# Kernel optimization log

Hardware: AMD Instinct MI355X
Metric: run time of the kernel (lower is better)

Reference implementation:

```python
import jax, jax.numpy as jnp
import numpy as np
import math

D = 1024
DFF = 4 * D
EPS = 1e-5

def layer_norm(x, g, b):
    mu = jnp.mean(x, axis=-1, keepdims=True)
    var = jnp.mean(jnp.square(x - mu), axis=-1, keepdims=True)
    return (x - mu) * jax.lax.rsqrt(var + EPS) * g + b

def setup_inputs() -> dict:
    key = jax.random.key(0)
    ks = jax.random.split(key, 12)
    s = 1.0 / math.sqrt(D)
    x = jax.random.normal(ks[0], (4, 2048, D), dtype=jnp.float32)
    Wq = jax.random.uniform(ks[1], (D, D), jnp.float32, -s, s)
    Wk = jax.random.uniform(ks[2], (D, D), jnp.float32, -s, s)
    Wv = jax.random.uniform(ks[3], (D, D), jnp.float32, -s, s)
    ln1_g = jnp.ones((D,), jnp.float32); ln1_b = jnp.zeros((D,), jnp.float32)
    ln2_g = jnp.ones((D,), jnp.float32); ln2_b = jnp.zeros((D,), jnp.float32)
    ff1_w = jax.random.uniform(ks[4], (D, DFF), jnp.float32, -s, s)
    ff1_b = jax.random.uniform(ks[5], (DFF,), jnp.float32, -s, s)
    s2 = 1.0 / math.sqrt(DFF)
    ff2_w = jax.random.uniform(ks[6], (DFF, D), jnp.float32, -s2, s2)
    ff2_b = jax.random.uniform(ks[7], (D,), jnp.float32, -s2, s2)
    return {"x": x, "Wq": Wq, "Wk": Wk, "Wv": Wv,
            "ln1_g": ln1_g, "ln1_b": ln1_b, "ln2_g": ln2_g, "ln2_b": ln2_b,
            "ff1_w": ff1_w, "ff1_b": ff1_b, "ff2_w": ff2_w, "ff2_b": ff2_b}

def reference(x, Wq, Wk, Wv, ln1_g, ln1_b, ln2_g, ln2_b, ff1_w, ff1_b, ff2_w, ff2_b):
    B, S, d = x.shape
    Q = x @ Wq  # [B,S,D]
    K = x @ Wk
    V = x @ Wv
    scores = jnp.einsum('bsd,btd->bst', Q, K) / math.sqrt(d)
    causal = jnp.tril(jnp.ones((S, S), dtype=bool))  # [S,S]
    scores = jnp.where(causal, scores, -jnp.inf)
    attn = jax.nn.softmax(scores, axis=-1)
    attn_out = jnp.einsum('bst,btd->bsd', attn, V)
    h = layer_norm(x + attn_out, ln1_g, ln1_b)
    ff = (jax.nn.gelu(h @ ff1_w + ff1_b, approximate=False)) @ ff2_w + ff2_b
    return layer_norm(h + ff, ln2_g, ln2_b)
```

## Files before the change

kernel.cpp:

```cpp
#include <hip/hip_runtime.h>
#include <math.h>


#define D_MODEL 1024
#define DFF_    4096
#define SEQ_    2048
#define NBATCH  4

typedef unsigned short u16;
typedef __attribute__((ext_vector_type(8))) short bf16x8;
typedef __attribute__((ext_vector_type(4))) float f32x4;

__device__ __forceinline__ u16 f2bf(float f) {
    unsigned u = __float_as_uint(f);
    unsigned r = (u + 0x7fffu + ((u >> 16) & 1u)) >> 16;
    return (u16)r;
}
__device__ __forceinline__ float bf2f(u16 h) {
    return __uint_as_float(((unsigned)h) << 16);
}

__device__ __forceinline__ void gld_lds16(const void* g, void* l) {
#if __has_builtin(__builtin_amdgcn_global_load_lds)
    typedef __attribute__((address_space(1))) const unsigned int as1_u32;
    typedef __attribute__((address_space(3))) unsigned int as3_u32;
    __builtin_amdgcn_global_load_lds((as1_u32*)g, (as3_u32*)l, 16, 0, 0);
#else
    *(bf16x8*)l = *(const bf16x8*)g;
#endif
}

constexpr int BMt = 128, BNt = 128, BKt = 32;

template <int CAUSAL, int EPI, int OUT, int SWZ_HS>
__global__ __launch_bounds__(256)
void mfma_gemm(const u16* __restrict__ Ah, const u16* __restrict__ Al,
               const u16* __restrict__ Bh, const u16* __restrict__ Bl,
               float* __restrict__ Cf, u16* __restrict__ Ch, u16* __restrict__ Cl,
               const float* __restrict__ bias, const float* __restrict__ resid,
               int M, int N, int K, long bA, long bB, long bC, float alpha)
{
    const int z = blockIdx.z;
    int bx = blockIdx.x, by = blockIdx.y;
    if (SWZ_HS > 0) {
        const int GX = gridDim.x, GY = gridDim.y;
        const int g   = bx + GX * by;
        const int xcd = g & 7;
        const int li  = g >> 3;
        const int RB  = GY >> 3;
        const int r   = li % SWZ_HS;
        const int c   = (li / SWZ_HS) % GX;
        const int s   = li / (SWZ_HS * GX);
        by = xcd * RB + s * SWZ_HS + r;
        bx = c;
    }
    const int rowStart = by * BMt;
    const int colStart = bx * BNt;
    if (CAUSAL == 1 && colStart >= rowStart + BMt) return;

    const u16* Ah_ = Ah + bA * z;
    const u16* Al_ = Al + bA * z;
    const u16* Bh_ = Bh + bB * z;
    const u16* Bl_ = Bl + bB * z;

    __shared__ __align__(16) u16 AsH[128][32];
    __shared__ __align__(16) u16 AsL[128][32];
    __shared__ __align__(16) u16 BsH[128][32];
    __shared__ __align__(16) u16 BsL[128][32];

    const int tid = threadIdx.x;
    const int l   = tid & 63;
    const int w   = tid >> 6;
    const int wr  = w >> 1, wc = w & 1;
    const int fr  = l & 15;
    const int fk  = (l >> 4) * 8;

    const f32x4 fz = {0.f, 0.f, 0.f, 0.f};
    f32x4 acc[4][4];
#pragma unroll
    for (int m = 0; m < 4; ++m)
#pragma unroll
        for (int n = 0; n < 4; ++n) acc[m][n] = fz;

    int kTiles = K / BKt;
    if (CAUSAL == 2) {
        int kEnd = rowStart + BMt;
        if (kEnd > K) kEnd = K;
        kTiles = kEnd / BKt;
    }

    for (int t = 0; t < kTiles; ++t) {
        const int kb = t * BKt;
#pragma unroll
        for (int s = 0; s < 2; ++s) {
            int gg = s * 256 + tid;
            int r  = gg >> 2;
            int ko = (gg & 3) * 8;
            size_t aoff = (size_t)(rowStart + r) * K + kb + ko;
            size_t boff = (size_t)(colStart + r) * K + kb + ko;
            gld_lds16(Ah_ + aoff, &AsH[0][0] + (size_t)gg * 8);
            gld_lds16(Al_ + aoff, &AsL[0][0] + (size_t)gg * 8);
            gld_lds16(Bh_ + boff, &BsH[0][0] + (size_t)gg * 8);
            gld_lds16(Bl_ + boff, &BsL[0][0] + (size_t)gg * 8);
        }
        __syncthreads();

        bf16x8 aH[4], aL[4], bH[4], bL[4];
#pragma unroll
        for (int m = 0; m < 4; ++m) {
            aH[m] = *(const bf16x8*)&AsH[wr * 64 + m * 16 + fr][fk];
            aL[m] = *(const bf16x8*)&AsL[wr * 64 + m * 16 + fr][fk];
        }
#pragma unroll
        for (int n = 0; n < 4; ++n) {
            bH[n] = *(const bf16x8*)&BsH[wc * 64 + n * 16 + fr][fk];
            bL[n] = *(const bf16x8*)&BsL[wc * 64 + n * 16 + fr][fk];
        }
#pragma unroll
        for (int m = 0; m < 4; ++m)
#pragma unroll
            for (int n = 0; n < 4; ++n) {
                acc[m][n] = __builtin_amdgcn_mfma_f32_16x16x32_bf16(aH[m], bH[n], acc[m][n], 0, 0, 0);
                acc[m][n] = __builtin_amdgcn_mfma_f32_16x16x32_bf16(aH[m], bL[n], acc[m][n], 0, 0, 0);
                acc[m][n] = __builtin_amdgcn_mfma_f32_16x16x32_bf16(aL[m], bH[n], acc[m][n], 0, 0, 0);
            }
        __syncthreads();
    }

#pragma unroll
    for (int m = 0; m < 4; ++m) {
#pragma unroll
        for (int n = 0; n < 4; ++n) {
            const int col = colStart + wc * 64 + n * 16 + fr;
            float bv = 0.f;
            if (EPI >= 1) bv = bias[col];
#pragma unroll
            for (int r = 0; r < 4; ++r) {
                const int row = rowStart + wr * 64 + m * 16 + (l >> 4) * 4 + r;
                float v = acc[m][n][r] * alpha;
                if (EPI >= 1) v += bv;
                if (EPI == 2) v = 0.5f * v * (1.0f + erff(v * 0.70710678118654752f));
                if (EPI == 3) v += resid[(size_t)row * N + col];
                if (OUT == 0) {
                    Cf[bC * z + (size_t)row * N + col] = v;
                } else if (OUT == 1) {
                    size_t o = bC * z + (size_t)row * N + col;
                    u16 h = f2bf(v);
                    Ch[o] = h;
                    Cl[o] = f2bf(v - bf2f(h));
                } else {
                    int b = row >> 11, tt = row & (SEQ_ - 1);
                    size_t o = ((size_t)b << 21) + ((size_t)col << 11) + tt;
                    u16 h = f2bf(v);
                    Ch[o] = h;
                    Cl[o] = f2bf(v - bf2f(h));
                }
            }
        }
    }
}

__global__ __launch_bounds__(256)
void split_f32(const float* __restrict__ in, u16* __restrict__ oh, u16* __restrict__ ol, long n4)
{
    long i  = (long)blockIdx.x * 256 + threadIdx.x;
    long st = (long)gridDim.x * 256;
    for (; i < n4; i += st) {
        float4 v = ((const float4*)in)[i];
        ushort4 h, lo;
        h.x = f2bf(v.x); lo.x = f2bf(v.x - bf2f(h.x));
        h.y = f2bf(v.y); lo.y = f2bf(v.y - bf2f(h.y));
        h.z = f2bf(v.z); lo.z = f2bf(v.z - bf2f(h.z));
        h.w = f2bf(v.w); lo.w = f2bf(v.w - bf2f(h.w));
        ((ushort4*)oh)[i] = h;
        ((ushort4*)ol)[i] = lo;
    }
}

__global__ __launch_bounds__(256)
void transpose_split(const float* __restrict__ in, u16* __restrict__ oh, u16* __restrict__ ol,
                     int R, int C)
{
    __shared__ float t[32][33];
    const int c0 = blockIdx.x * 32, r0 = blockIdx.y * 32;
    const int tx = threadIdx.x, ty = threadIdx.y;
#pragma unroll
    for (int s = 0; s < 4; ++s)
        t[ty + s * 8][tx] = in[(size_t)(r0 + ty + s * 8) * C + c0 + tx];
    __syncthreads();
#pragma unroll
    for (int s = 0; s < 4; ++s) {
        int cl = ty + s * 8;
        float v = t[tx][cl];
        size_t o = (size_t)(c0 + cl) * R + r0 + tx;
        u16 h = f2bf(v);
        oh[o] = h;
        ol[o] = f2bf(v - bf2f(h));
    }
}

__global__ __launch_bounds__(256)
void softmax_split(u16* __restrict__ hi, u16* __restrict__ lo)
{
    const int row = blockIdx.x;
    const int b   = row >> 11;
    const int i   = row & (SEQ_ - 1);
    u16* ph = hi + ((size_t)b * SEQ_ + i) * SEQ_;
    u16* pl = lo + ((size_t)b * SEQ_ + i) * SEQ_;
    const int len = i + 1;
    const int lenPad = (len + 127) & ~127;
    const int tid = threadIdx.x;
    __shared__ float buf[SEQ_];
    __shared__ float red[256];

    float m = -INFINITY;
    for (int j = tid; j < len; j += 256) {
        float s = bf2f(ph[j]) + bf2f(pl[j]);
        buf[j] = s;
        m = fmaxf(m, s);
    }
    red[tid] = m; __syncthreads();
    for (int o = 128; o > 0; o >>= 1) { if (tid < o) red[tid] = fmaxf(red[tid], red[tid + o]); __syncthreads(); }
    m = red[0]; __syncthreads();

    float sum = 0.f;
    for (int j = tid; j < len; j += 256) { float e = expf(buf[j] - m); buf[j] = e; sum += e; }
    red[tid] = sum; __syncthreads();
    for (int o = 128; o > 0; o >>= 1) { if (tid < o) red[tid] += red[tid + o]; __syncthreads(); }
    const float inv = 1.0f / red[0];

    for (int j = tid; j < len; j += 256) {
        float p = buf[j] * inv;
        u16 h = f2bf(p);
        ph[j] = h;
        pl[j] = f2bf(p - bf2f(h));
    }
    for (int j = len + tid; j < lenPad; j += 256) { ph[j] = 0; pl[j] = 0; }
}

__global__ __launch_bounds__(256)
void ln_kernel(const float* __restrict__ a, const float* __restrict__ r,
               const float* __restrict__ g, const float* __restrict__ beta,
               float* __restrict__ out, u16* __restrict__ oh, u16* __restrict__ ol)
{
    const int row = blockIdx.x, tid = threadIdx.x;
    float4 v = ((const float4*)(a + (size_t)row * D_MODEL))[tid];
    if (r) {
        float4 wv = ((const float4*)(r + (size_t)row * D_MODEL))[tid];
        v.x += wv.x; v.y += wv.y; v.z += wv.z; v.w += wv.w;
    }
    __shared__ float red[256];
    red[tid] = v.x + v.y + v.z + v.w; __syncthreads();
    for (int o = 128; o > 0; o >>= 1) { if (tid < o) red[tid] += red[tid + o]; __syncthreads(); }
    const float mu = red[0] * (1.0f / D_MODEL);
    __syncthreads();
    const float dx = v.x - mu, dy = v.y - mu, dz = v.z - mu, dw = v.w - mu;
    red[tid] = dx * dx + dy * dy + dz * dz + dw * dw; __syncthreads();
    for (int o = 128; o > 0; o >>= 1) { if (tid < o) red[tid] += red[tid + o]; __syncthreads(); }
    const float rs = rsqrtf(red[0] * (1.0f / D_MODEL) + 1e-5f);
    const float4 gv = ((const float4*)g)[tid];
    const float4 bv = ((const float4*)beta)[tid];
    float4 o4 = make_float4(dx * rs * gv.x + bv.x, dy * rs * gv.y + bv.y,
                            dz * rs * gv.z + bv.z, dw * rs * gv.w + bv.w);
    ((float4*)(out + (size_t)row * D_MODEL))[tid] = o4;
    if (oh) {
        ushort4 h, lo;
        h.x = f2bf(o4.x); lo.x = f2bf(o4.x - bf2f(h.x));
        h.y = f2bf(o4.y); lo.y = f2bf(o4.y - bf2f(h.y));
        h.z = f2bf(o4.z); lo.z = f2bf(o4.z - bf2f(h.z));
        h.w = f2bf(o4.w); lo.w = f2bf(o4.w - bf2f(h.w));
        ((ushort4*)(oh + (size_t)row * D_MODEL))[tid] = h;
        ((ushort4*)(ol + (size_t)row * D_MODEL))[tid] = lo;
    }
}

extern "C" void kernel_launch(void* const* d_in, const int* in_sizes, int n_in,
                              void* d_out, int out_size, void* d_ws, size_t ws_size,
                              hipStream_t stream)
{
    const float* x    = (const float*)d_in[0];
    const float* Wq   = (const float*)d_in[1];
    const float* Wk   = (const float*)d_in[2];
    const float* Wv   = (const float*)d_in[3];
    const float* ln1g = (const float*)d_in[4];
    const float* ln1b = (const float*)d_in[5];
    const float* ln2g = (const float*)d_in[6];
    const float* ln2b = (const float*)d_in[7];
    const float* W1   = (const float*)d_in[8];
    const float* b1   = (const float*)d_in[9];
    const float* W2   = (const float*)d_in[10];
    const float* b2   = (const float*)d_in[11];

    const int Mrows = NBATCH * SEQ_;

    char* wsb = (char*)d_ws;
    auto U = [&](size_t mb) { return (u16*)(wsb + mb * (size_t)(1 << 20)); };
    u16 *WqTh = U(0),   *WqTl = U(2);
    u16 *WkTh = U(4),   *WkTl = U(6);
    u16 *WvTh = U(8),   *WvTl = U(10);
    u16 *xsh  = U(12),  *xsl  = U(28);
    float* attn = (float*)(wsb + 12 * (size_t)(1 << 20));
    u16 *W1Th = U(12),  *W1Tl = U(20);
    u16 *W2Th = U(28),  *W2Tl = U(36);
    u16 *Qsh  = U(44),  *Qsl  = U(60);
    u16 *hsh  = U(44),  *hsl  = U(60);
    u16 *Ksh  = U(76),  *Ksl  = U(92);
    u16 *Vth  = U(108), *Vtl  = U(124);
    u16 *Ssh  = U(140), *Ssl  = U(172);
    u16 *fh   = U(76),  *fl   = U(140);
    float* h  = (float*)d_out;

    dim3 b256(256), tb(32, 8);

    transpose_split<<<dim3(32, 32), tb, 0, stream>>>(Wq, WqTh, WqTl, 1024, 1024);
    transpose_split<<<dim3(32, 32), tb, 0, stream>>>(Wk, WkTh, WkTl, 1024, 1024);
    transpose_split<<<dim3(32, 32), tb, 0, stream>>>(Wv, WvTh, WvTl, 1024, 1024);
    split_f32<<<dim3(2048), b256, 0, stream>>>(x, xsh, xsl, (long)Mrows * D_MODEL / 4);

    mfma_gemm<0, 0, 1, 4><<<dim3(8, 64, 1), b256, 0, stream>>>(
        xsh, xsl, WqTh, WqTl, nullptr, Qsh, Qsl, nullptr, nullptr,
        Mrows, D_MODEL, D_MODEL, 0, 0, 0, 1.f);
    mfma_gemm<0, 0, 1, 4><<<dim3(8, 64, 1), b256, 0, stream>>>(
        xsh, xsl, WkTh, WkTl, nullptr, Ksh, Ksl, nullptr, nullptr,
        Mrows, D_MODEL, D_MODEL, 0, 0, 0, 1.f);
    mfma_gemm<0, 0, 2, 4><<<dim3(8, 64, 1), b256, 0, stream>>>(
        xsh, xsl, WvTh, WvTl, nullptr, Vth, Vtl, nullptr, nullptr,
        Mrows, D_MODEL, D_MODEL, 0, 0, 0, 1.f);

    mfma_gemm<1, 0, 1, 0><<<dim3(16, 16, NBATCH), b256, 0, stream>>>(
        Qsh, Qsl, Ksh, Ksl, nullptr, Ssh, Ssl, nullptr, nullptr,
        SEQ_, SEQ_, D_MODEL, (long)SEQ_ * D_MODEL, (long)SEQ_ * D_MODEL,
        (long)SEQ_ * SEQ_, 0.03125f);
    softmax_split<<<dim3(Mrows), b256, 0, stream>>>(Ssh, Ssl);

    mfma_gemm<2, 0, 0, 0><<<dim3(8, 16, NBATCH), b256, 0, stream>>>(
        Ssh, Ssl, Vth, Vtl, attn, nullptr, nullptr, nullptr, nullptr,
        SEQ_, D_MODEL, SEQ_, (long)SEQ_ * SEQ_, (long)D_MODEL * SEQ_,
        (long)SEQ_ * D_MODEL, 1.f);

    ln_kernel<<<dim3(Mrows), b256, 0, stream>>>(x, attn, ln1g, ln1b, h, hsh, hsl);

    transpose_split<<<dim3(128, 32), tb, 0, stream>>>(W1, W1Th, W1Tl, 1024, 4096);
    transpose_split<<<dim3(32, 128), tb, 0, stream>>>(W2, W2Th, W2Tl, 4096, 1024);

    mfma_gemm<0, 2, 1, 4><<<dim3(32, 64, 1), b256, 0, stream>>>(
        hsh, hsl, W1Th, W1Tl, nullptr, fh, fl, b1, nullptr,
        Mrows, DFF_, D_MODEL, 0, 0, 0, 1.f);

    mfma_gemm<0, 3, 0, 1><<<dim3(8, 64, 1), b256, 0, stream>>>(
        fh, fl, W2Th, W2Tl, (float*)d_out, nullptr, nullptr, b2, h,
        Mrows, D_MODEL, DFF_, 0, 0, 0, 1.f);

    ln_kernel<<<dim3(Mrows), b256, 0, stream>>>(
        (const float*)d_out, nullptr, ln2g, ln2b, (float*)d_out, nullptr, nullptr);
}
```

Baseline: 1.038 ms.

## Add 512-thread 128x256 triple-buffered ping-pong GEMM for projection and FFN matmuls

Adds a new GEMM kernel with 512 threads, 128x256 tiles, and a three-stage LDS ring filled by direct global-to-LDS loads. Each K step is split into two halves whose staging is interleaved with MFMA bursts under raised wave priority. The kernel replaces the old GEMM for the Q/K/V projections and both FFN matmuls, aiming to hide memory latency and raise MFMA utilisation. It uses 144KB of LDS with two blocks per CU requested, which risks limiting occupancy and adds barrier overhead.

Result: faster. 949.8 us (-8.5%).

```diff
diff --git a/kernel.cpp b/kernel.cpp
--- a/kernel.cpp
+++ b/kernel.cpp
@@ -48,11 +48,11 @@
         const int xcd = g & 7;
         const int li  = g >> 3;
         const int RB  = GY >> 3;
-        const int r   = li % SWZ_HS;
-        const int c   = (li / SWZ_HS) % GX;
-        const int s   = li / (SWZ_HS * GX);
-        by = xcd * RB + s * SWZ_HS + r;
-        bx = c;
+        const int rr_ = li % SWZ_HS;
+        const int cc_ = (li / SWZ_HS) % GX;
+        const int ss_ = li / (SWZ_HS * GX);
+        by = xcd * RB + ss_ * SWZ_HS + rr_;
+        bx = cc_;
     }
     const int rowStart = by * BMt;
     const int colStart = bx * BNt;
@@ -145,6 +145,174 @@
                     Cf[bC * z + (size_t)row * N + col] = v;
                 } else if (OUT == 1) {
                     size_t o = bC * z + (size_t)row * N + col;
+                    u16 h = f2bf(v);
+                    Ch[o] = h;
+                    Cl[o] = f2bf(v - bf2f(h));
+                } else {
+                    int b = row >> 11, tt = row & (SEQ_ - 1);
+                    size_t o = ((size_t)b << 21) + ((size_t)col << 11) + tt;
+                    u16 h = f2bf(v);
+                    Ch[o] = h;
+                    Cl[o] = f2bf(v - bf2f(h));
+                }
+            }
+        }
+    }
+}
+
+template <int EPI, int OUT, int SWZ_HS>
+__global__ __launch_bounds__(512, 2)
+void mfma_gemm_ps(const u16* __restrict__ Ah, const u16* __restrict__ Al,
+                  const u16* __restrict__ Bh, const u16* __restrict__ Bl,
+                  float* __restrict__ Cf, u16* __restrict__ Ch, u16* __restrict__ Cl,
+                  const float* __restrict__ bias, const float* __restrict__ resid,
+                  int M, int N, int K, float alpha)
+{
+    int bx = blockIdx.x, by = blockIdx.y;
+    if (SWZ_HS > 0) {
+        const int GX = gridDim.x, GY = gridDim.y;
+        const int g   = bx + GX * by;
+        const int xcd = g & 7;
+        const int li  = g >> 3;
+        const int RB  = GY >> 3;
+        const int rr_ = li % SWZ_HS;
+        const int cc_ = (li / SWZ_HS) % GX;
+        const int ss_ = li / (SWZ_HS * GX);
+        by = xcd * RB + ss_ * SWZ_HS + rr_;
+        bx = cc_;
+    }
+    const int rowStart = by * 128;
+    const int colStart = bx * 256;
+
+    __shared__ __align__(16) char lds[3 * 49152];
+
+    const int tid = threadIdx.x;
+    const int l  = tid & 63;
+    const int w  = tid >> 6;
+    const int wr = w >> 2;
+    const int wc = w & 3;
+    const int fr = l & 15;
+    const int ck = l >> 4;
+
+    const int T = K >> 5;
+
+    const f32x4 fz = {0.f, 0.f, 0.f, 0.f};
+    f32x4 acc[4][4];
+#pragma unroll
+    for (int m = 0; m < 4; ++m)
+#pragma unroll
+        for (int n = 0; n < 4; ++n) acc[m][n] = fz;
+
+    auto stage_g = [&](const u16* __restrict__ src, int rowBase, int g,
+                       char* region, int kb) {
+        int row = g >> 2, cp = g & 3;
+        int ko  = (cp ^ ((row >> 1) & 3)) << 3;
+        gld_lds16(src + (size_t)(rowBase + row) * K + kb + ko, region + g * 16);
+    };
+    auto rd = [&](const char* region, int row) -> bf16x8 {
+        return *(const bf16x8*)(region + row * 64 + ((ck ^ ((row >> 1) & 3)) << 4));
+    };
+
+    {
+        char* b0 = lds;
+        char* b1 = lds + 49152;
+        stage_g(Ah, rowStart, tid,       b0 + 0,     0);
+        stage_g(Al, rowStart, tid,       b0 + 8192,  0);
+        stage_g(Bh, colStart, tid,       b0 + 16384, 0);
+        stage_g(Bh, colStart, tid + 512, b0 + 16384, 0);
+        stage_g(Bl, colStart, tid,       b0 + 32768, 0);
+        stage_g(Bl, colStart, tid + 512, b0 + 32768, 0);
+        stage_g(Ah, rowStart, tid,       b1 + 0,     32);
+        stage_g(Al, rowStart, tid,       b1 + 8192,  32);
+        stage_g(Bh, colStart, tid,       b1 + 16384, 32);
+        stage_g(Bh, colStart, tid + 512, b1 + 16384, 32);
+        stage_g(Bl, colStart, tid,       b1 + 32768, 32);
+        stage_g(Bl, colStart, tid + 512, b1 + 32768, 32);
+    }
+    asm volatile("s_waitcnt vmcnt(6)" ::: "memory");
+    __builtin_amdgcn_s_barrier();
+
+    for (int t = 0; t < T; ++t) {
+        const char* cb = lds + (t % 3) * 49152;
+        char*       sb = lds + ((t + 2) % 3) * 49152;
+        const bool  doStage = (t + 2) < T;
+        const int   kb2 = (t + 2) << 5;
+
+        bf16x8 aH[4], aL[4];
+#pragma unroll
+        for (int m = 0; m < 4; ++m) {
+            aH[m] = rd(cb + 0,    wr * 64 + m * 16 + fr);
+            aL[m] = rd(cb + 8192, wr * 64 + m * 16 + fr);
+        }
+        bf16x8 bH0 = rd(cb + 16384, wc * 64 + 0 * 16 + fr);
+        bf16x8 bH1 = rd(cb + 16384, wc * 64 + 1 * 16 + fr);
+        bf16x8 bL0 = rd(cb + 32768, wc * 64 + 0 * 16 + fr);
+        bf16x8 bL1 = rd(cb + 32768, wc * 64 + 1 * 16 + fr);
+        if (doStage) {
+            stage_g(Ah, rowStart, tid, sb + 0,     kb2);
+            stage_g(Al, rowStart, tid, sb + 8192,  kb2);
+            stage_g(Bh, colStart, tid, sb + 16384, kb2);
+        }
+        __builtin_amdgcn_s_barrier();
+        asm volatile("s_waitcnt lgkmcnt(0)" ::: "memory");
+        __builtin_amdgcn_s_setprio(1);
+#pragma unroll
+        for (int m = 0; m < 4; ++m) {
+            acc[m][0] = __builtin_amdgcn_mfma_f32_16x16x32_bf16(aH[m], bH0, acc[m][0], 0, 0, 0);
+            acc[m][0] = __builtin_amdgcn_mfma_f32_16x16x32_bf16(aH[m], bL0, acc[m][0], 0, 0, 0);
+            acc[m][0] = __builtin_amdgcn_mfma_f32_16x16x32_bf16(aL[m], bH0, acc[m][0], 0, 0, 0);
+            acc[m][1] = __builtin_amdgcn_mfma_f32_16x16x32_bf16(aH[m], bH1, acc[m][1], 0, 0, 0);
+            acc[m][1] = __builtin_amdgcn_mfma_f32_16x16x32_bf16(aH[m], bL1, acc[m][1], 0, 0, 0);
+            acc[m][1] = __builtin_amdgcn_mfma_f32_16x16x32_bf16(aL[m], bH1, acc[m][1], 0, 0, 0);
+        }
+        __builtin_amdgcn_s_setprio(0);
+        __builtin_amdgcn_s_barrier();
+
+        bf16x8 bH2 = rd(cb + 16384, wc * 64 + 2 * 16 + fr);
+        bf16x8 bH3 = rd(cb + 16384, wc * 64 + 3 * 16 + fr);
+        bf16x8 bL2 = rd(cb + 32768, wc * 64 + 2 * 16 + fr);
+        bf16x8 bL3 = rd(cb + 32768, wc * 64 + 3 * 16 + fr);
+        if (doStage) {
+            stage_g(Bh, colStart, tid + 512, sb + 16384, kb2);
+            stage_g(Bl, colStart, tid,       sb + 32768, kb2);
+            stage_g(Bl, colStart, tid + 512, sb + 32768, kb2);
+        }
+        __builtin_amdgcn_s_barrier();
+        asm volatile("s_waitcnt lgkmcnt(0)" ::: "memory");
+        __builtin_amdgcn_s_setprio(1);
+#pragma unroll
+        for (int m = 0; m < 4; ++m) {
+            acc[m][2] = __builtin_amdgcn_mfma_f32_16x16x32_bf16(aH[m], bH2, acc[m][2], 0, 0, 0);
+            acc[m][2] = __builtin_amdgcn_mfma_f32_16x16x32_bf16(aH[m], bL2, acc[m][2], 0, 0, 0);
+            acc[m][2] = __builtin_amdgcn_mfma_f32_16x16x32_bf16(aL[m], bH2, acc[m][2], 0, 0, 0);
+            acc[m][3] = __builtin_amdgcn_mfma_f32_16x16x32_bf16(aH[m], bH3, acc[m][3], 0, 0, 0);
+            acc[m][3] = __builtin_amdgcn_mfma_f32_16x16x32_bf16(aH[m], bL3, acc[m][3], 0, 0, 0);
+            acc[m][3] = __builtin_amdgcn_mfma_f32_16x16x32_bf16(aL[m], bH3, acc[m][3], 0, 0, 0);
+        }
+        __builtin_amdgcn_s_setprio(0);
+        if (doStage) asm volatile("s_waitcnt vmcnt(6)" ::: "memory");
+        else         asm volatile("s_waitcnt vmcnt(0)" ::: "memory");
+        __builtin_amdgcn_s_barrier();
+    }
+
+#pragma unroll
+    for (int m = 0; m < 4; ++m) {
+#pragma unroll
+        for (int n = 0; n < 4; ++n) {
+            const int col = colStart + wc * 64 + n * 16 + fr;
+            float bv = 0.f;
+            if (EPI >= 1) bv = bias[col];
+#pragma unroll
+            for (int rr = 0; rr < 4; ++rr) {
+                const int row = rowStart + wr * 64 + m * 16 + (l >> 4) * 4 + rr;
+                float v = acc[m][n][rr] * alpha;
+                if (EPI >= 1) v += bv;
+                if (EPI == 2) v = 0.5f * v * (1.0f + erff(v * 0.70710678118654752f));
+                if (EPI == 3) v += resid[(size_t)row * N + col];
+                if (OUT == 0) {
+                    Cf[(size_t)row * N + col] = v;
+                } else if (OUT == 1) {
+                    size_t o = (size_t)row * N + col;
                     u16 h = f2bf(v);
                     Ch[o] = h;
                     Cl[o] = f2bf(v - bf2f(h));
@@ -310,22 +478,22 @@
     u16 *fh   = U(76),  *fl   = U(140);
     float* h  = (float*)d_out;
 
-    dim3 b256(256), tb(32, 8);
+    dim3 b256(256), b512(512), tb(32, 8);
 
     transpose_split<<<dim3(32, 32), tb, 0, stream>>>(Wq, WqTh, WqTl, 1024, 1024);
     transpose_split<<<dim3(32, 32), tb, 0, stream>>>(Wk, WkTh, WkTl, 1024, 1024);
     transpose_split<<<dim3(32, 32), tb, 0, stream>>>(Wv, WvTh, WvTl, 1024, 1024);
     split_f32<<<dim3(2048), b256, 0, stream>>>(x, xsh, xsl, (long)Mrows * D_MODEL / 4);
 
-    mfma_gemm<0, 0, 1, 4><<<dim3(8, 64, 1), b256, 0, stream>>>(
+    mfma_gemm_ps<0, 1, 4><<<dim3(4, 64), b512, 0, stream>>>(
         xsh, xsl, WqTh, WqTl, nullptr, Qsh, Qsl, nullptr, nullptr,
-        Mrows, D_MODEL, D_MODEL, 0, 0, 0, 1.f);
-    mfma_gemm<0, 0, 1, 4><<<dim3(8, 64, 1), b256, 0, stream>>>(
+        Mrows, D_MODEL, D_MODEL, 1.f);
+    mfma_gemm_ps<0, 1, 4><<<dim3(4, 64), b512, 0, stream>>>(
         xsh, xsl, WkTh, WkTl, nullptr, Ksh, Ksl, nullptr, nullptr,
-        Mrows, D_MODEL, D_MODEL, 0, 0, 0, 1.f);
-    mfma_gemm<0, 0, 2, 4><<<dim3(8, 64, 1), b256, 0, stream>>>(
+        Mrows, D_MODEL, D_MODEL, 1.f);
+    mfma_gemm_ps<0, 2, 4><<<dim3(4, 64), b512, 0, stream>>>(
         xsh, xsl, WvTh, WvTl, nullptr, Vth, Vtl, nullptr, nullptr,
-        Mrows, D_MODEL, D_MODEL, 0, 0, 0, 1.f);
+        Mrows, D_MODEL, D_MODEL, 1.f);
 
     mfma_gemm<1, 0, 1, 0><<<dim3(16, 16, NBATCH), b256, 0, stream>>>(
         Qsh, Qsl, Ksh, Ksl, nullptr, Ssh, Ssl, nullptr, nullptr,
@@ -343,13 +511,13 @@
     transpose_split<<<dim3(128, 32), tb, 0, stream>>>(W1, W1Th, W1Tl, 1024, 4096);
     transpose_split<<<dim3(32, 128), tb, 0, stream>>>(W2, W2Th, W2Tl, 4096, 1024);
 
-    mfma_gemm<0, 2, 1, 4><<<dim3(32, 64, 1), b256, 0, stream>>>(
+    mfma_gemm_ps<2, 1, 4><<<dim3(16, 64), b512, 0, stream>>>(
         hsh, hsl, W1Th, W1Tl, nullptr, fh, fl, b1, nullptr,
-        Mrows, DFF_, D_MODEL, 0, 0, 0, 1.f);
-
-    mfma_gemm<0, 3, 0, 1><<<dim3(8, 64, 1), b256, 0, stream>>>(
+        Mrows, DFF_, D_MODEL, 1.f);
+
+    mfma_gemm_ps<3, 0, 1><<<dim3(4, 64), b512, 0, stream>>>(
         fh, fl, W2Th, W2Tl, (float*)d_out, nullptr, nullptr, b2, h,
-        Mrows, D_MODEL, DFF_, 0, 0, 0, 1.f);
+        Mrows, D_MODEL, DFF_, 1.f);
 
     ln_kernel<<<dim3(Mrows), b256, 0, stream>>>(
         (const float*)d_out, nullptr, ln2g, ln2b, (float*)d_out, nullptr, nullptr);
```

## Triple-buffer GEMM LDS tiles with swizzled layout and wider 128x256 blocks

Applied to the files above, without the earlier changes.

Rewrites the split-bf16 MFMA GEMM to use 512-thread blocks computing 128x256 tiles, with a three-stage LDS ring prefetching two k-tiles ahead via direct global-to-LDS loads and vmcnt-based waits instead of full syncthreads. LDS rows are XOR-swizzled to cut bank conflicts on fragment reads, and B fragments are loaded in two halves to lower register pressure. The aim is to hide global load latency and raise MFMA utilisation. In exchange it uses 144KB of LDS, limiting occupancy to one block per CU, and halves the grid size.

Measured after the change: 919.8 us. 1.13x faster.

```diff
diff --git a/kernel.cpp b/kernel.cpp
--- a/kernel.cpp
+++ b/kernel.cpp
@@ -30,15 +30,13 @@
 #endif
 }
 
-constexpr int BMt = 128, BNt = 128, BKt = 32;
-
 template <int CAUSAL, int EPI, int OUT, int SWZ_HS>
-__global__ __launch_bounds__(256)
-void mfma_gemm(const u16* __restrict__ Ah, const u16* __restrict__ Al,
-               const u16* __restrict__ Bh, const u16* __restrict__ Bl,
-               float* __restrict__ Cf, u16* __restrict__ Ch, u16* __restrict__ Cl,
-               const float* __restrict__ bias, const float* __restrict__ resid,
-               int M, int N, int K, long bA, long bB, long bC, float alpha)
+__global__ __launch_bounds__(512)
+void mfma_gemm_ps(const u16* __restrict__ Ah, const u16* __restrict__ Al,
+                  const u16* __restrict__ Bh, const u16* __restrict__ Bl,
+                  float* __restrict__ Cf, u16* __restrict__ Ch, u16* __restrict__ Cl,
+                  const float* __restrict__ bias, const float* __restrict__ resid,
+                  int N, int K, long bA, long bB, long bC, float alpha)
 {
     const int z = blockIdx.z;
     int bx = blockIdx.x, by = blockIdx.y;
@@ -48,32 +46,37 @@
         const int xcd = g & 7;
         const int li  = g >> 3;
         const int RB  = GY >> 3;
-        const int r   = li % SWZ_HS;
-        const int c   = (li / SWZ_HS) % GX;
-        const int s   = li / (SWZ_HS * GX);
-        by = xcd * RB + s * SWZ_HS + r;
-        bx = c;
-    }
-    const int rowStart = by * BMt;
-    const int colStart = bx * BNt;
-    if (CAUSAL == 1 && colStart >= rowStart + BMt) return;
+        const int rr_ = li % SWZ_HS;
+        const int cc_ = (li / SWZ_HS) % GX;
+        const int ss_ = li / (SWZ_HS * GX);
+        by = xcd * RB + ss_ * SWZ_HS + rr_;
+        bx = cc_;
+    }
+    const int rowStart = by * 128;
+    const int colStart = bx * 256;
+    if (CAUSAL == 1 && colStart >= rowStart + 128) return;
 
     const u16* Ah_ = Ah + bA * z;
     const u16* Al_ = Al + bA * z;
     const u16* Bh_ = Bh + bB * z;
     const u16* Bl_ = Bl + bB * z;
 
-    __shared__ __align__(16) u16 AsH[128][32];
-    __shared__ __align__(16) u16 AsL[128][32];
-    __shared__ __align__(16) u16 BsH[128][32];
-    __shared__ __align__(16) u16 BsL[128][32];
+    __shared__ __align__(16) char lds[3 * 49152];
 
     const int tid = threadIdx.x;
-    const int l   = tid & 63;
-    const int w   = tid >> 6;
-    const int wr  = w >> 1, wc = w & 1;
-    const int fr  = l & 15;
-    const int fk  = (l >> 4) * 8;
+    const int l  = tid & 63;
+    const int w  = tid >> 6;
+    const int wr = w >> 2;
+    const int wc = w & 3;
+    const int fr = l & 15;
+    const int ck = l >> 4;
+
+    int T = K >> 5;
+    if (CAUSAL == 2) {
+        int kEnd = rowStart + 128;
+        if (kEnd > K) kEnd = K;
+        T = kEnd >> 5;
+    }
 
     const f32x4 fz = {0.f, 0.f, 0.f, 0.f};
     f32x4 acc[4][4];
@@ -82,49 +85,88 @@
 #pragma unroll
         for (int n = 0; n < 4; ++n) acc[m][n] = fz;
 
-    int kTiles = K / BKt;
-    if (CAUSAL == 2) {
-        int kEnd = rowStart + BMt;
-        if (kEnd > K) kEnd = K;
-        kTiles = kEnd / BKt;
-    }
-
-    for (int t = 0; t < kTiles; ++t) {
-        const int kb = t * BKt;
-#pragma unroll
-        for (int s = 0; s < 2; ++s) {
-            int gg = s * 256 + tid;
-            int r  = gg >> 2;
-            int ko = (gg & 3) * 8;
-            size_t aoff = (size_t)(rowStart + r) * K + kb + ko;
-            size_t boff = (size_t)(colStart + r) * K + kb + ko;
-            gld_lds16(Ah_ + aoff, &AsH[0][0] + (size_t)gg * 8);
-            gld_lds16(Al_ + aoff, &AsL[0][0] + (size_t)gg * 8);
-            gld_lds16(Bh_ + boff, &BsH[0][0] + (size_t)gg * 8);
-            gld_lds16(Bl_ + boff, &BsL[0][0] + (size_t)gg * 8);
-        }
-        __syncthreads();
-
-        bf16x8 aH[4], aL[4], bH[4], bL[4];
+    auto stage_g = [&](const u16* __restrict__ src, int rowBase, int g,
+                       char* region, int kb) {
+        int row = g >> 2, cp = g & 3;
+        int ko  = (cp ^ ((row >> 1) & 3)) << 3;
+        gld_lds16(src + (size_t)(rowBase + row) * K + kb + ko, region + g * 16);
+    };
+    auto rd = [&](const char* region, int row) -> bf16x8 {
+        return *(const bf16x8*)(region + row * 64 + ((ck ^ ((row >> 1) & 3)) << 4));
+    };
+
+    {
+        char* b0 = lds;
+        char* b1 = lds + 49152;
+        stage_g(Ah_, rowStart, tid,       b0 + 0,     0);
+        stage_g(Al_, rowStart, tid,       b0 + 8192,  0);
+        stage_g(Bh_, colStart, tid,       b0 + 16384, 0);
+        stage_g(Bh_, colStart, tid + 512, b0 + 16384, 0);
+        stage_g(Bl_, colStart, tid,       b0 + 32768, 0);
+        stage_g(Bl_, colStart, tid + 512, b0 + 32768, 0);
+        stage_g(Ah_, rowStart, tid,       b1 + 0,     32);
+        stage_g(Al_, rowStart, tid,       b1 + 8192,  32);
+        stage_g(Bh_, colStart, tid,       b1 + 16384, 32);
+        stage_g(Bh_, colStart, tid + 512, b1 + 16384, 32);
+        stage_g(Bl_, colStart, tid,       b1 + 32768, 32);
+        stage_g(Bl_, colStart, tid + 512, b1 + 32768, 32);
+    }
+    asm volatile("s_waitcnt vmcnt(6)" ::: "memory");
+    __builtin_amdgcn_s_barrier();
+    __builtin_amdgcn_sched_barrier(0);
+
+    for (int t = 0; t < T; ++t) {
+        const char* cb = lds + (t % 3) * 49152;
+        char*       sb = lds + ((t + 2) % 3) * 49152;
+        const bool  doStage = (t + 2) < T;
+        const int   kb2 = (t + 2) << 5;
+
+        if (doStage) {
+            stage_g(Ah_, rowStart, tid,       sb + 0,     kb2);
+            stage_g(Al_, rowStart, tid,       sb + 8192,  kb2);
+            stage_g(Bh_, colStart, tid,       sb + 16384, kb2);
+            stage_g(Bh_, colStart, tid + 512, sb + 16384, kb2);
+            stage_g(Bl_, colStart, tid,       sb + 32768, kb2);
+            stage_g(Bl_, colStart, tid + 512, sb + 32768, kb2);
+        }
+
+        bf16x8 aH[4], aL[4];
 #pragma unroll
         for (int m = 0; m < 4; ++m) {
-            aH[m] = *(const bf16x8*)&AsH[wr * 64 + m * 16 + fr][fk];
-            aL[m] = *(const bf16x8*)&AsL[wr * 64 + m * 16 + fr][fk];
-        }
-#pragma unroll
-        for (int n = 0; n < 4; ++n) {
-            bH[n] = *(const bf16x8*)&BsH[wc * 64 + n * 16 + fr][fk];
-            bL[n] = *(const bf16x8*)&BsL[wc * 64 + n * 16 + fr][fk];
-        }
-#pragma unroll
-        for (int m = 0; m < 4; ++m)
-#pragma unroll
-            for (int n = 0; n < 4; ++n) {
-                acc[m][n] = __builtin_amdgcn_mfma_f32_16x16x32_bf16(aH[m], bH[n], acc[m][n], 0, 0, 0);
-                acc[m][n] = __builtin_amdgcn_mfma_f32_16x16x32_bf16(aH[m], bL[n], acc[m][n], 0, 0, 0);
-                acc[m][n] = __builtin_amdgcn_mfma_f32_16x16x32_bf16(aL[m], bH[n], acc[m][n], 0, 0, 0);
-            }
-        __syncthreads();
+            aH[m] = rd(cb + 0,    wr * 64 + m * 16 + fr);
+            aL[m] = rd(cb + 8192, wr * 64 + m * 16 + fr);
+        }
+        bf16x8 bH0 = rd(cb + 16384, wc * 64 + 0 * 16 + fr);
+        bf16x8 bH1 = rd(cb + 16384, wc * 64 + 1 * 16 + fr);
+        bf16x8 bL0 = rd(cb + 32768, wc * 64 + 0 * 16 + fr);
+        bf16x8 bL1 = rd(cb + 32768, wc * 64 + 1 * 16 + fr);
+#pragma unroll
+        for (int m = 0; m < 4; ++m) {
+            acc[m][0] = __builtin_amdgcn_mfma_f32_16x16x32_bf16(aH[m], bH0, acc[m][0], 0, 0, 0);
+            acc[m][0] = __builtin_amdgcn_mfma_f32_16x16x32_bf16(aH[m], bL0, acc[m][0], 0, 0, 0);
+            acc[m][0] = __builtin_amdgcn_mfma_f32_16x16x32_bf16(aL[m], bH0, acc[m][0], 0, 0, 0);
+            acc[m][1] = __builtin_amdgcn_mfma_f32_16x16x32_bf16(aH[m], bH1, acc[m][1], 0, 0, 0);
+            acc[m][1] = __builtin_amdgcn_mfma_f32_16x16x32_bf16(aH[m], bL1, acc[m][1], 0, 0, 0);
+            acc[m][1] = __builtin_amdgcn_mfma_f32_16x16x32_bf16(aL[m], bH1, acc[m][1], 0, 0, 0);
+        }
+        bf16x8 bH2 = rd(cb + 16384, wc * 64 + 2 * 16 + fr);
+        bf16x8 bH3 = rd(cb + 16384, wc * 64 + 3 * 16 + fr);
+        bf16x8 bL2 = rd(cb + 32768, wc * 64 + 2 * 16 + fr);
+        bf16x8 bL3 = rd(cb + 32768, wc * 64 + 3 * 16 + fr);
+#pragma unroll
+        for (int m = 0; m < 4; ++m) {
+            acc[m][2] = __builtin_amdgcn_mfma_f32_16x16x32_bf16(aH[m], bH2, acc[m][2], 0, 0, 0);
+            acc[m][2] = __builtin_amdgcn_mfma_f32_16x16x32_bf16(aH[m], bL2, acc[m][2], 0, 0, 0);
+            acc[m][2] = __builtin_amdgcn_mfma_f32_16x16x32_bf16(aL[m], bH2, acc[m][2], 0, 0, 0);
+            acc[m][3] = __builtin_amdgcn_mfma_f32_16x16x32_bf16(aH[m], bH3, acc[m][3], 0, 0, 0);
+            acc[m][3] = __builtin_amdgcn_mfma_f32_16x16x32_bf16(aH[m], bL3, acc[m][3], 0, 0, 0);
+            acc[m][3] = __builtin_amdgcn_mfma_f32_16x16x32_bf16(aL[m], bH3, acc[m][3], 0, 0, 0);
+        }
+
+        if (doStage) asm volatile("s_waitcnt vmcnt(6)" ::: "memory");
+        else         asm volatile("s_waitcnt vmcnt(0)" ::: "memory");
+        __builtin_amdgcn_s_barrier();
+        __builtin_amdgcn_sched_barrier(0);
     }
 
 #pragma unroll
@@ -135,9 +177,9 @@
             float bv = 0.f;
             if (EPI >= 1) bv = bias[col];
 #pragma unroll
-            for (int r = 0; r < 4; ++r) {
-                const int row = rowStart + wr * 64 + m * 16 + (l >> 4) * 4 + r;
-                float v = acc[m][n][r] * alpha;
+            for (int rr = 0; rr < 4; ++rr) {
+                const int row = rowStart + wr * 64 + m * 16 + (l >> 4) * 4 + rr;
+                float v = acc[m][n][rr] * alpha;
                 if (EPI >= 1) v += bv;
                 if (EPI == 2) v = 0.5f * v * (1.0f + erff(v * 0.70710678118654752f));
                 if (EPI == 3) v += resid[(size_t)row * N + col];
@@ -310,32 +352,32 @@
     u16 *fh   = U(76),  *fl   = U(140);
     float* h  = (float*)d_out;
 
-    dim3 b256(256), tb(32, 8);
+    dim3 b256(256), b512(512), tb(32, 8);
 
     transpose_split<<<dim3(32, 32), tb, 0, stream>>>(Wq, WqTh, WqTl, 1024, 1024);
     transpose_split<<<dim3(32, 32), tb, 0, stream>>>(Wk, WkTh, WkTl, 1024, 1024);
     transpose_split<<<dim3(32, 32), tb, 0, stream>>>(Wv, WvTh, WvTl, 1024, 1024);
     split_f32<<<dim3(2048), b256, 0, stream>>>(x, xsh, xsl, (long)Mrows * D_MODEL / 4);
 
-    mfma_gemm<0, 0, 1, 4><<<dim3(8, 64, 1), b256, 0, stream>>>(
+    mfma_gemm_ps<0, 0, 1, 4><<<dim3(4, 64), b512, 0, stream>>>(
         xsh, xsl, WqTh, WqTl, nullptr, Qsh, Qsl, nullptr, nullptr,
-        Mrows, D_MODEL, D_MODEL, 0, 0, 0, 1.f);
-    mfma_gemm<0, 0, 1, 4><<<dim3(8, 64, 1), b256, 0, stream>>>(
+        D_MODEL, D_MODEL, 0, 0, 0, 1.f);
+    mfma_gemm_ps<0, 0, 1, 4><<<dim3(4, 64), b512, 0, stream>>>(
         xsh, xsl, WkTh, WkTl, nullptr, Ksh, Ksl, nullptr, nullptr,
-        Mrows, D_MODEL, D_MODEL, 0, 0, 0, 1.f);
-    mfma_gemm<0, 0, 2, 4><<<dim3(8, 64, 1), b256, 0, stream>>>(
+        D_MODEL, D_MODEL, 0, 0, 0, 1.f);
+    mfma_gemm_ps<0, 0, 2, 4><<<dim3(4, 64), b512, 0, stream>>>(
         xsh, xsl, WvTh, WvTl, nullptr, Vth, Vtl, nullptr, nullptr,
-        Mrows, D_MODEL, D_MODEL, 0, 0, 0, 1.f);
-
-    mfma_gemm<1, 0, 1, 0><<<dim3(16, 16, NBATCH), b256, 0, stream>>>(
+        D_MODEL, D_MODEL, 0, 0, 0, 1.f);
+
+    mfma_gemm_ps<1, 0, 1, 0><<<dim3(8, 16, NBATCH), b512, 0, stream>>>(
         Qsh, Qsl, Ksh, Ksl, nullptr, Ssh, Ssl, nullptr, nullptr,
-        SEQ_, SEQ_, D_MODEL, (long)SEQ_ * D_MODEL, (long)SEQ_ * D_MODEL,
+        SEQ_, D_MODEL, (long)SEQ_ * D_MODEL, (long)SEQ_ * D_MODEL,
         (long)SEQ_ * SEQ_, 0.03125f);
     softmax_split<<<dim3(Mrows), b256, 0, stream>>>(Ssh, Ssl);
 
-    mfma_gemm<2, 0, 0, 0><<<dim3(8, 16, NBATCH), b256, 0, stream>>>(
+    mfma_gemm_ps<2, 0, 0, 0><<<dim3(4, 16, NBATCH), b512, 0, stream>>>(
         Ssh, Ssl, Vth, Vtl, attn, nullptr, nullptr, nullptr, nullptr,
-        SEQ_, D_MODEL, SEQ_, (long)SEQ_ * SEQ_, (long)D_MODEL * SEQ_,
+        D_MODEL, SEQ_, (long)SEQ_ * SEQ_, (long)D_MODEL * SEQ_,
         (long)SEQ_ * D_MODEL, 1.f);
 
     ln_kernel<<<dim3(Mrows), b256, 0, stream>>>(x, attn, ln1g, ln1b, h, hsh, hsl);
@@ -343,13 +385,13 @@
     transpose_split<<<dim3(128, 32), tb, 0, stream>>>(W1, W1Th, W1Tl, 1024, 4096);
     transpose_split<<<dim3(32, 128), tb, 0, stream>>>(W2, W2Th, W2Tl, 4096, 1024);
 
-    mfma_gemm<0, 2, 1, 4><<<dim3(32, 64, 1), b256, 0, stream>>>(
+    mfma_gemm_ps<0, 2, 1, 4><<<dim3(16, 64), b512, 0, stream>>>(
         hsh, hsl, W1Th, W1Tl, nullptr, fh, fl, b1, nullptr,
-        Mrows, DFF_, D_MODEL, 0, 0, 0, 1.f);
-
-    mfma_gemm<0, 3, 0, 1><<<dim3(8, 64, 1), b256, 0, stream>>>(
+        DFF_, D_MODEL, 0, 0, 0, 1.f);
+
+    mfma_gemm_ps<0, 3, 0, 1><<<dim3(4, 64), b512, 0, stream>>>(
         fh, fl, W2Th, W2Tl, (float*)d_out, nullptr, nullptr, b2, h,
-        Mrows, D_MODEL, DFF_, 0, 0, 0, 1.f);
+        D_MODEL, DFF_, 0, 0, 0, 1.f);
 
     ln_kernel<<<dim3(Mrows), b256, 0, stream>>>(
         (const float*)d_out, nullptr, ln2g, ln2b, (float*)d_out, nullptr, nullptr);
```
